# Kernel optimization log

Hardware: AMD Instinct MI355X
Metric: run time of the kernel (lower is better)

## Reference

```python
import jax, jax.numpy as jnp
import numpy as np
from jax import lax


def setup_inputs() -> dict:
    key = jax.random.key(0)
    k0, k1, k2, k3 = jax.random.split(key, 4)
    B, C, H, W = 16, 64, 192, 192
    K = 3
    x0 = jax.random.normal(k0, (B, C, H, W), dtype=jnp.float32)
    d = jax.random.normal(k1, (B, C), dtype=jnp.float32)
    w1 = jax.random.normal(k2, (C, C), dtype=jnp.float32) * 0.05
    w2 = jax.random.normal(k3, (C * K * K, C), dtype=jnp.float32) * 0.05
    return {"x0": x0, "d": d, "w1": w1, "w2": w2}


def reference(x0, d, w1, w2):
    b, c, h, w = x0.shape
    k = int(round((w2.shape[0] // c) ** 0.5))  # kernel_size
    # kernel-generating MLP: Linear(C,C,bias=False) -> LeakyReLU(0.1) -> Linear(C,C*k*k,bias=False)
    hid = jax.nn.leaky_relu(d @ w1.T, negative_slope=0.1)          # (B, C)
    ker = (hid @ w2.T).reshape(b * c, 1, k, k)                      # (B*C, 1, k, k)
    pad = (k - 1) // 2
    # per-(batch,channel) dynamic depthwise conv: groups = B*C
    out = lax.conv_general_dilated(
        x0.reshape(1, b * c, h, w),
        ker,
        window_strides=(1, 1),
        padding=[(pad, pad), (pad, pad)],
        dimension_numbers=("NCHW", "OIHW", "NCHW"),
        feature_group_count=b * c,
    )
    return out.reshape(b, c, h, w)
```

## Files before the change

kernel.cpp:

```cpp
#include <hip/hip_runtime.h>


#define BB 16
#define CC 64
#define HH 192
#define WW 192
#define KERLEN (CC * 9)
#define QW (WW / 4)
#define RPT 4
#define TPP (QW * (HH / RPT))
#define BPP (TPP / 256)

typedef float f4 __attribute__((ext_vector_type(4)));

__global__ __launch_bounds__(256) void gen_kernels(
    const float* __restrict__ d,
    const float* __restrict__ w1,
    const float* __restrict__ w2,
    float* __restrict__ ker)
{
    __shared__ float dd[CC];
    __shared__ float hid[CC];
    const int b = blockIdx.x;
    const int t = threadIdx.x;

    if (t < CC) dd[t] = d[b * CC + t];
    __syncthreads();

    if (t < CC) {
        const float* w1r = w1 + t * CC;
        float acc = 0.f;
        #pragma unroll 8
        for (int m = 0; m < CC; ++m) acc += dd[m] * w1r[m];
        hid[t] = acc > 0.f ? acc : 0.1f * acc;
    }
    __syncthreads();

    for (int o = t; o < KERLEN; o += 256) {
        const float* w2r = w2 + o * CC;
        float acc = 0.f;
        #pragma unroll 8
        for (int k = 0; k < CC; ++k) acc += hid[k] * w2r[k];
        ker[b * KERLEN + o] = acc;
    }
}

__global__ __launch_bounds__(256, 8) void dconv3x3_v4(
    const float* __restrict__ x,
    const float* __restrict__ ker,
    float* __restrict__ out)
{
    const int blk = blockIdx.x;
    const int bc  = blk / BPP;
    const int sub = blk - bc * BPP;

    const float* kp = ker + bc * 9;
    const float k00 = kp[0], k01 = kp[1], k02 = kp[2];
    const float k10 = kp[3], k11 = kp[4], k12 = kp[5];
    const float k20 = kp[6], k21 = kp[7], k22 = kp[8];

    const int task = sub * 256 + threadIdx.x;
    const int rg   = task / QW;
    const int qw   = task - rg * QW;
    const int w    = qw * 4;
    const int r0   = rg * RPT;

    const bool hasL = (qw > 0);
    const bool hasR = (qw < QW - 1);
    const int  offL = hasL ? -1 : 0;
    const int  offR = hasR ?  4 : 0;

    const float* __restrict__ xp = x   + (size_t)bc * HH * WW + w;
    float* __restrict__       op = out + (size_t)bc * HH * WW + w;

    f4    c[RPT + 2];
    float l[RPT + 2], r[RPT + 2];
    const f4 zero = {0.f, 0.f, 0.f, 0.f};

    #pragma unroll
    for (int j = 0; j < RPT + 2; ++j) {
        const int rr  = r0 - 1 + j;
        const int rcl = rr < 0 ? 0 : (rr >= HH ? HH - 1 : rr);
        const float* p = xp + rcl * WW;
        const f4 v     = *(const f4*)p;
        const float lv = p[offL];
        const float rv = p[offR];
        const bool ok  = (rr >= 0) & (rr < HH);
        c[j] = ok ? v : zero;
        l[j] = (ok && hasL) ? lv : 0.f;
        r[j] = (ok && hasR) ? rv : 0.f;
    }

    #pragma unroll
    for (int i = 0; i < RPT; ++i) {
        const f4 ca = c[i], cb = c[i + 1], cd = c[i + 2];
        const float la = l[i], lb = l[i + 1], lc = l[i + 2];
        const float ra = r[i], rb = r[i + 1], rc = r[i + 2];

        f4 o;
        o.x = k00 * la   + k01 * ca.x + k02 * ca.y
            + k10 * lb   + k11 * cb.x + k12 * cb.y
            + k20 * lc   + k21 * cd.x + k22 * cd.y;
        o.y = k00 * ca.x + k01 * ca.y + k02 * ca.z
            + k10 * cb.x + k11 * cb.y + k12 * cb.z
            + k20 * cd.x + k21 * cd.y + k22 * cd.z;
        o.z = k00 * ca.y + k01 * ca.z + k02 * ca.w
            + k10 * cb.y + k11 * cb.z + k12 * cb.w
            + k20 * cd.y + k21 * cd.z + k22 * cd.w;
        o.w = k00 * ca.z + k01 * ca.w + k02 * ra
            + k10 * cb.z + k11 * cb.w + k12 * rb
            + k20 * cd.z + k21 * cd.w + k22 * rc;

        __builtin_nontemporal_store(o, (f4*)(op + (size_t)(r0 + i) * WW));
    }
}

extern "C" void kernel_launch(void* const* d_in, const int* in_sizes, int n_in,
                              void* d_out, int out_size, void* d_ws, size_t ws_size,
                              hipStream_t stream) {
    const float* x0 = (const float*)d_in[0];
    const float* d  = (const float*)d_in[1];
    const float* w1 = (const float*)d_in[2];
    const float* w2 = (const float*)d_in[3];
    float* out = (float*)d_out;
    float* ker = (float*)d_ws;

    gen_kernels<<<BB, 256, 0, stream>>>(d, w1, w2, ker);
    dconv3x3_v4<<<BB * CC * BPP, 256, 0, stream>>>(x0, ker, out);
}
```

Measured before the change: 270.3 us.

## Stage 34-row input tiles into LDS via direct global-to-LDS loads

The depthwise conv kernel now gives each block a 32-row tile of one channel plane. It loads the 34-row halo tile into shared memory with global_load_lds 16-byte transfers, then computes 2 rows per task from LDS over 3 task rounds. This replaces the per-thread overlapping global reads (a 6-row halo per 4 output rows plus scalar side loads), which cuts redundant global and L2 traffic. In exchange it adds a full wait and barrier with no overlap, uses about 28KB of LDS per block, lowers the launch-bounds occupancy hint, and makes the grid much smaller.

```diff
diff --git a/kernel.cpp b/kernel.cpp
--- a/kernel.cpp
+++ b/kernel.cpp
@@ -7,9 +7,12 @@
 #define WW 192
 #define KERLEN (CC * 9)
 #define QW (WW / 4)
-#define RPT 4
-#define TPP (QW * (HH / RPT))
-#define BPP (TPP / 256)
+#define ROWS 32
+#define RIN (ROWS + 2)
+#define ROWB (WW * 4)
+#define TILEB (RIN * ROWB)
+#define STAGEB (7 * 4096)
+#define TILES (HH / ROWS)
 
 typedef float f4 __attribute__((ext_vector_type(4)));
 
@@ -45,73 +48,100 @@
     }
 }
 
-__global__ __launch_bounds__(256, 8) void dconv3x3_v4(
+__device__ __forceinline__ void gload_lds16(const float* g, float* l) {
+    __builtin_amdgcn_global_load_lds(
+        (const __attribute__((address_space(1))) unsigned int*)g,
+        (__attribute__((address_space(3))) unsigned int*)l,
+        16, 0, 0);
+}
+
+__global__ __launch_bounds__(256, 5) void dconv3x3_v5(
     const float* __restrict__ x,
     const float* __restrict__ ker,
     float* __restrict__ out)
 {
-    const int blk = blockIdx.x;
-    const int bc  = blk / BPP;
-    const int sub = blk - bc * BPP;
+    __shared__ __align__(16) float lds[STAGEB / 4];
+
+    const int blk  = blockIdx.x;
+    const int bc   = blk / TILES;
+    const int tile = blk - bc * TILES;
+    const int r0   = tile * ROWS;
+
+    const float* __restrict__ xp = x   + (size_t)bc * HH * WW;
+    float* __restrict__       op = out + (size_t)bc * HH * WW;
 
     const float* kp = ker + bc * 9;
     const float k00 = kp[0], k01 = kp[1], k02 = kp[2];
     const float k10 = kp[3], k11 = kp[4], k12 = kp[5];
     const float k20 = kp[6], k21 = kp[7], k22 = kp[8];
 
-    const int task = sub * 256 + threadIdx.x;
-    const int rg   = task / QW;
-    const int qw   = task - rg * QW;
-    const int w    = qw * 4;
-    const int r0   = rg * RPT;
+    const int t = threadIdx.x;
 
-    const bool hasL = (qw > 0);
-    const bool hasR = (qw < QW - 1);
-    const int  offL = hasL ? -1 : 0;
-    const int  offR = hasR ?  4 : 0;
+    #pragma unroll
+    for (int i = 0; i < 7; ++i) {
+        const int idx  = i * 4096 + t * 16;
+        const int j    = idx / ROWB;
+        const int colb = idx - j * ROWB;
+        int srow = r0 - 1 + j;
+        srow = srow < 0 ? 0 : (srow > HH - 1 ? HH - 1 : srow);
+        gload_lds16(xp + srow * WW + (colb >> 2), lds + (idx >> 2));
+    }
+    asm volatile("s_waitcnt vmcnt(0)" ::: "memory");
+    __syncthreads();
 
-    const float* __restrict__ xp = x   + (size_t)bc * HH * WW + w;
-    float* __restrict__       op = out + (size_t)bc * HH * WW + w;
-
-    f4    c[RPT + 2];
-    float l[RPT + 2], r[RPT + 2];
     const f4 zero = {0.f, 0.f, 0.f, 0.f};
 
     #pragma unroll
-    for (int j = 0; j < RPT + 2; ++j) {
-        const int rr  = r0 - 1 + j;
-        const int rcl = rr < 0 ? 0 : (rr >= HH ? HH - 1 : rr);
-        const float* p = xp + rcl * WW;
-        const f4 v     = *(const f4*)p;
-        const float lv = p[offL];
-        const float rv = p[offR];
-        const bool ok  = (rr >= 0) & (rr < HH);
-        c[j] = ok ? v : zero;
-        l[j] = (ok && hasL) ? lv : 0.f;
-        r[j] = (ok && hasR) ? rv : 0.f;
-    }
+    for (int k2 = 0; k2 < 3; ++k2) {
+        const int task = t + k2 * 256;
+        const int pr   = task / QW;
+        const int q    = task - pr * QW;
+        const int lr0  = pr * 2;
 
-    #pragma unroll
-    for (int i = 0; i < RPT; ++i) {
-        const f4 ca = c[i], cb = c[i + 1], cd = c[i + 2];
-        const float la = l[i], lb = l[i + 1], lc = l[i + 2];
-        const float ra = r[i], rb = r[i + 1], rc = r[i + 2];
+        const bool hasL = (q > 0);
+        const bool hasR = (q < QW - 1);
+        const int  offL = hasL ? -1 : 0;
+        const int  offR = hasR ?  4 : 0;
 
-        f4 o;
-        o.x = k00 * la   + k01 * ca.x + k02 * ca.y
-            + k10 * lb   + k11 * cb.x + k12 * cb.y
-            + k20 * lc   + k21 * cd.x + k22 * cd.y;
-        o.y = k00 * ca.x + k01 * ca.y + k02 * ca.z
-            + k10 * cb.x + k11 * cb.y + k12 * cb.z
-            + k20 * cd.x + k21 * cd.y + k22 * cd.z;
-        o.z = k00 * ca.y + k01 * ca.z + k02 * ca.w
-            + k10 * cb.y + k11 * cb.z + k12 * cb.w
-            + k20 * cd.y + k21 * cd.z + k22 * cd.w;
-        o.w = k00 * ca.z + k01 * ca.w + k02 * ra
-            + k10 * cb.z + k11 * cb.w + k12 * rb
-            + k20 * cd.z + k21 * cd.w + k22 * rc;
+        f4    c[4];
+        float l[4], r[4];
 
-        __builtin_nontemporal_store(o, (f4*)(op + (size_t)(r0 + i) * WW));
+        #pragma unroll
+        for (int dj = 0; dj < 4; ++dj) {
+            const int g = r0 + lr0 - 1 + dj;
+            const float* p = lds + (lr0 + dj) * WW + q * 4;
+            const f4 v     = *(const f4*)p;
+            const float lv = p[offL];
+            const float rv = p[offR];
+            const bool ok  = (unsigned)g < (unsigned)HH;
+            c[dj] = ok ? v : zero;
+            l[dj] = (ok && hasL) ? lv : 0.f;
+            r[dj] = (ok && hasR) ? rv : 0.f;
+        }
+
+        #pragma unroll
+        for (int i = 0; i < 2; ++i) {
+            const f4 ca = c[i], cb = c[i + 1], cd = c[i + 2];
+            const float la = l[i], lb = l[i + 1], lc = l[i + 2];
+            const float ra = r[i], rb = r[i + 1], rc = r[i + 2];
+
+            f4 o;
+            o.x = k00 * la   + k01 * ca.x + k02 * ca.y
+                + k10 * lb   + k11 * cb.x + k12 * cb.y
+                + k20 * lc   + k21 * cd.x + k22 * cd.y;
+            o.y = k00 * ca.x + k01 * ca.y + k02 * ca.z
+                + k10 * cb.x + k11 * cb.y + k12 * cb.z
+                + k20 * cd.x + k21 * cd.y + k22 * cd.z;
+            o.z = k00 * ca.y + k01 * ca.z + k02 * ca.w
+                + k10 * cb.y + k11 * cb.z + k12 * cb.w
+                + k20 * cd.y + k21 * cd.z + k22 * cd.w;
+            o.w = k00 * ca.z + k01 * ca.w + k02 * ra
+                + k10 * cb.z + k11 * cb.w + k12 * rb
+                + k20 * cd.z + k21 * cd.w + k22 * rc;
+
+            __builtin_nontemporal_store(
+                o, (f4*)(op + (size_t)(r0 + lr0 + i) * WW + q * 4));
+        }
     }
 }
 
@@ -126,5 +156,5 @@
     float* ker = (float*)d_ws;
 
     gen_kernels<<<BB, 256, 0, stream>>>(d, w1, w2, ker);
-    dconv3x3_v4<<<BB * CC * BPP, 256, 0, stream>>>(x0, ker, out);
+    dconv3x3_v5<<<BB * CC * TILES, 256, 0, stream>>>(x0, ker, out);
 }
```

Result: no change. 272.2 us (+0.7%).
